# Optimization experiments

Measured on AMD Instinct MI355X. Metric: run time of the kernel, lower is better.

Reference implementation:

```python
import jax, jax.numpy as jnp
import numpy as np

N, E, B = 50000, 400000, 8
ND, ED, H, L = 32, 16, 128, 3

def setup_inputs() -> dict:
    key = jax.random.key(0)
    ks = jax.random.split(key, 32)
    s = 0.05
    inp = {
        'x': jax.random.normal(ks[0], (N, ND), jnp.float32),
        'edge_attr': jax.random.normal(ks[1], (E, ED), jnp.float32),
        'global_feature': jax.random.normal(ks[2], (B, 1), jnp.float32),
        'edge_index': jax.random.randint(ks[3], (2, E), 0, N, jnp.int64),
        'batch': jnp.sort(jax.random.randint(ks[4], (N,), 0, B, jnp.int64)),
        # embeddings
        'Wn': jax.random.normal(ks[5], (ND, H), jnp.float32) * s,
        'bn': jnp.zeros((H,), jnp.float32),
        'We': jax.random.normal(ks[6], (ED, H), jnp.float32) * s,
        'be': jnp.zeros((H,), jnp.float32),
        'Wg': jax.random.normal(ks[7], (1, H), jnp.float32) * s,
        'bg': jnp.zeros((H,), jnp.float32),
        # message-passing layers (stacked over L)
        'mW1': jax.random.normal(ks[8], (L, 3 * H, H), jnp.float32) * s,
        'mb1': jnp.zeros((L, H), jnp.float32),
        'mW2': jax.random.normal(ks[9], (L, H, H), jnp.float32) * s,
        'mb2': jnp.zeros((L, H), jnp.float32),
        'uW1': jax.random.normal(ks[10], (L, 2 * H, H), jnp.float32) * s,
        'ub1': jnp.zeros((L, H), jnp.float32),
        'uW2': jax.random.normal(ks[11], (L, H, H), jnp.float32) * s,
        'ub2': jnp.zeros((L, H), jnp.float32),
        # readout MLP
        'rW1': jax.random.normal(ks[12], (2 * H, H), jnp.float32) * s,
        'rb1': jnp.zeros((H,), jnp.float32),
        'rW2': jax.random.normal(ks[13], (H, H // 2), jnp.float32) * s,
        'rb2': jnp.zeros((H // 2,), jnp.float32),
        'rW3': jax.random.normal(ks[14], (H // 2, 1), jnp.float32) * s,
        'rb3': jnp.zeros((1,), jnp.float32),
    }
    return inp

def reference(x, edge_attr, global_feature, Wn, bn, We, be, Wg, bg,
              mW1, mb1, mW2, mb2, uW1, ub1, uW2, ub2,
              rW1, rb1, rW2, rb2, rW3, rb3, edge_index, batch):
    h = x @ Wn + bn                      # [N,H]
    e = edge_attr @ We + be              # [E,H]
    g = global_feature @ Wg + bg         # [B,H]
    src, dst = edge_index[0], edge_index[1]  # PyG: x_j=source, x_i=target, aggregate at target
    for l in range(L):
        m_in = jnp.concatenate([h[dst], h[src], e], axis=1)            # [E,3H]
        m = jax.nn.relu(m_in @ mW1[l] + mb1[l]) @ mW2[l] + mb2[l]       # [E,H]
        aggr = jax.ops.segment_sum(m, dst, num_segments=N)              # [N,H]
        u_in = jnp.concatenate([h, aggr], axis=1)                       # [N,2H]
        upd = jax.nn.relu(u_in @ uW1[l] + ub1[l]) @ uW2[l] + ub2[l]
        h = h + upd
    counts = jax.ops.segment_sum(jnp.ones((N,), h.dtype), batch, num_segments=B)
    pooled = jax.ops.segment_sum(h, batch, num_segments=B) / jnp.maximum(counts, 1.0)[:, None]
    final = jnp.concatenate([pooled, g], axis=1)                        # [B,2H]
    out = jax.nn.relu(final @ rW1 + rb1)
    out = jax.nn.relu(out @ rW2 + rb2)
    return out @ rW3 + rb3                                              # [B,1]
```

## Files before the change

kernel.cpp:

```cpp
#include <hip/hip_runtime.h>

#define NN 50000
#define NPAD 50048
#define NE 400000
#define NBATCH 8
#define NDIM 32
#define EDIM 16
#define H 128
#define NLAYERS 3
#define CHUNK_ELEMS 4096
#define NODE_CHUNKS 24
#define ZW_CHUNK 8192
#define NSB 196
#define ZEB 128

#define EMB_B 1563
#define DEG_B 1563
#define ZWB (NLAYERS * 8)
#define WEFB NLAYERS
#define WUB (NLAYERS * 257)
#define P1_B (EMB_B + DEG_B + ZWB + WEFB + WUB)
#define K2_B (NSB + NLAYERS + NLAYERS * NODE_CHUNKS)
#define ZDZS_B (NPAD / 64)
#define ZE_B (NE / ZEB)
#define ZZ_B (ZDZS_B + ZE_B)

typedef __attribute__((ext_vector_type(8))) __bf16 bf16x8;
typedef __attribute__((ext_vector_type(16))) float f32x16;
typedef __attribute__((ext_vector_type(8))) short short8;
typedef __attribute__((ext_vector_type(2))) float v2f;

__device__ __forceinline__ void block_sync_lds() {
  asm volatile("s_waitcnt lgkmcnt(0)\ns_barrier" ::: "memory");
}
__device__ __forceinline__ v2f bf2f(unsigned u) {
  v2f r;
  r.x = __uint_as_float(u << 16);
  r.y = __uint_as_float(u & 0xffff0000u);
  return r;
}

__global__ __launch_bounds__(256) void p1_kernel(
    const float* __restrict__ x, const float* __restrict__ Wn,
    const float* __restrict__ bn, __bf16* __restrict__ hb,
    const int* __restrict__ ei, int* __restrict__ deg,
    const float* __restrict__ mW1, __bf16* __restrict__ ZW,
    const float* __restrict__ mb1, const float* __restrict__ We,
    const float* __restrict__ be, float* __restrict__ Wef,
    float* __restrict__ bm, const float* __restrict__ uW1,
    const float* __restrict__ mW2, const float* __restrict__ mb2,
    float* __restrict__ Wu, float* __restrict__ va) {
  __shared__ __align__(16) float smem[NDIM * H + 32 * NDIM];
  int bi = blockIdx.x;
  int tid = threadIdx.x;
  if (bi < EMB_B) {
    float* Ws = smem;
    float* xs = smem + NDIM * H;
    int nbase = bi * 32;
    for (int f = tid; f < NDIM * H; f += 256) Ws[f] = Wn[f];
    for (int f = tid; f < 32 * NDIM; f += 256) {
      int gi = nbase * NDIM + f;
      xs[f] = (gi < NN * NDIM) ? x[gi] : 0.f;
    }
    __syncthreads();
    int j = tid & 127, g = tid >> 7;
    float b = bn[j];
    for (int nn = 0; nn < 16; ++nn) {
      int node = nbase + g * 16 + nn;
      if (node < NN) {
        float acc = b;
#pragma unroll
        for (int k = 0; k < NDIM; ++k)
          acc = fmaf(xs[(g * 16 + nn) * NDIM + k], Ws[k * H + j], acc);
        hb[(size_t)node * H + j] = (__bf16)acc;
      }
    }
  } else if (bi < EMB_B + DEG_B) {
    int e = (bi - EMB_B) * 256 + tid;
    if (e < NE) atomicAdd(&deg[ei[NE + e]], 1);
  } else if (bi < EMB_B + DEG_B + ZWB) {
    int bb = bi - EMB_B - DEG_B;
    int l = bb / 8;
    int c = bb % 8;
    const float* w1 = mW1 + (size_t)l * 384 * H;
    __bf16* dst = ZW + ((size_t)l * 8 + c) * ZW_CHUNK;
    for (int it = 0; it < 32; it += 4) {
      float wv[4];
#pragma unroll
      for (int q = 0; q < 4; ++q) {
        int flat = (it + q) * 256 + tid;
        int j = flat & 7;
        int lane = (flat >> 3) & 63;
        int nt = (flat >> 9) & 7;
        int k = c * 16 + ((lane >> 5) << 3) + j;
        int n = nt * 32 + (lane & 31);
        wv[q] = (n < 128) ? w1[(size_t)k * H + n]
                          : w1[(size_t)(128 + k) * H + (n - 128)];
      }
#pragma unroll
      for (int q = 0; q < 4; ++q) {
        int flat = (it + q) * 256 + tid;
        int hilo = flat >> 12;
        __bf16 hi = (__bf16)wv[q];
        __bf16 lo = (__bf16)(wv[q] - (float)hi);
        dst[flat] = hilo ? lo : hi;
      }
    }
  } else if (bi < EMB_B + DEG_B + ZWB + WEFB) {
    int l = bi - (EMB_B + DEG_B + ZWB);
    float* WeS = smem;
    float* beS = smem + 2048;
    for (int f = tid; f < EDIM * H; f += 256) WeS[f] = We[f];
    if (tid < 128) beS[tid] = be[tid];
    __syncthreads();
    if (tid < 128) {
      int n = tid;
      const float* w1 = mW1 + (size_t)l * 384 * H + (size_t)256 * H + n;
      float acc[EDIM];
#pragma unroll
      for (int i = 0; i < EDIM; ++i) acc[i] = 0.f;
      float accb = 0.f;
      for (int c = 0; c < H; c += 4) {
        float w0 = w1[(size_t)(c + 0) * H];
        float w1v = w1[(size_t)(c + 1) * H];
        float w2 = w1[(size_t)(c + 2) * H];
        float w3 = w1[(size_t)(c + 3) * H];
        accb = fmaf(beS[c + 0], w0, accb);
        accb = fmaf(beS[c + 1], w1v, accb);
        accb = fmaf(beS[c + 2], w2, accb);
        accb = fmaf(beS[c + 3], w3, accb);
#pragma unroll
        for (int i = 0; i < EDIM; ++i) {
          acc[i] = fmaf(WeS[i * H + c + 0], w0, acc[i]);
          acc[i] = fmaf(WeS[i * H + c + 1], w1v, acc[i]);
          acc[i] = fmaf(WeS[i * H + c + 2], w2, acc[i]);
          acc[i] = fmaf(WeS[i * H + c + 3], w3, acc[i]);
        }
      }
#pragma unroll
      for (int i = 0; i < EDIM; ++i)
        Wef[((size_t)l * EDIM + i) * H + n] = acc[i];
      bm[l * H + n] = mb1[l * H + n] + accb;
    }
  } else {
    int bb = bi - (EMB_B + DEG_B + ZWB + WEFB);
    int l = bb / 257;
    int r = bb % 257;
    int j = tid & 127, hf = tid >> 7;
    const float* u1 = uW1 + (size_t)l * 256 * H;
    if (r < 128) {
      if (tid < 128) Wu[((size_t)l * 256 + r) * H + j] = u1[(size_t)r * H + j];
    } else {
      float* rowS = smem;
      float* redS = smem + 128;
      if (tid < 128)
        rowS[tid] = (r < 256) ? mW2[((size_t)l * H + (r - 128)) * H + tid]
                              : mb2[l * H + tid];
      __syncthreads();
      int cb = hf * 64;
      float s0 = 0.f, s1 = 0.f, s2 = 0.f, s3 = 0.f;
      for (int c = 0; c < 64; c += 4) {
        float a0 = u1[(size_t)(128 + cb + c + 0) * H + j];
        float a1 = u1[(size_t)(128 + cb + c + 1) * H + j];
        float a2 = u1[(size_t)(128 + cb + c + 2) * H + j];
        float a3 = u1[(size_t)(128 + cb + c + 3) * H + j];
        s0 = fmaf(rowS[cb + c + 0], a0, s0);
        s1 = fmaf(rowS[cb + c + 1], a1, s1);
        s2 = fmaf(rowS[cb + c + 2], a2, s2);
        s3 = fmaf(rowS[cb + c + 3], a3, s3);
      }
      float s = (s0 + s1) + (s2 + s3);
      if (hf == 1) redS[j] = s;
      __syncthreads();
      if (hf == 0) {
        float tot = s + redS[j];
        if (r < 256) Wu[((size_t)l * 256 + r) * H + j] = tot;
        else va[l * H + j] = tot;
      }
    }
  }
}

__global__ __launch_bounds__(256) void k2_kernel(
    const int* __restrict__ deg, int* __restrict__ bsum,
    const float* __restrict__ Wef, __bf16* __restrict__ WefS,
    const float* __restrict__ Wu, const float* __restrict__ uW2,
    __bf16* __restrict__ WnS) {
  __shared__ int ws[4];
  int bi = blockIdx.x;
  int tid = threadIdx.x;
  if (bi < NSB) {
    int i = bi * 256 + tid;
    int lane = tid & 63, wid = tid >> 6;
    int v = (i < NN) ? deg[i] : 0;
#pragma unroll
    for (int off = 32; off; off >>= 1) v += __shfl_down(v, off);
    if (lane == 0) ws[wid] = v;
    __syncthreads();
    if (tid == 0) bsum[bi] = ws[0] + ws[1] + ws[2] + ws[3];
  } else if (bi < NSB + NLAYERS) {
    int l = bi - NSB;
    int nt = tid >> 6, lane = tid & 63;
    int n = nt * 32 + (lane & 31);
    int half = lane >> 5;
    const float* wl = Wef + (size_t)l * EDIM * H;
    __bf16* dst = WefS + (size_t)l * CHUNK_ELEMS;
#pragma unroll
    for (int j = 0; j < 8; ++j) {
      int k = half * 8 + j;
      float w = wl[(size_t)k * H + n];
      __bf16 hi = (__bf16)w;
      __bf16 lo = (__bf16)(w - (float)hi);
      dst[((0 * 4 + nt) * 64 + lane) * 8 + j] = hi;
      dst[((1 * 4 + nt) * 64 + lane) * 8 + j] = lo;
    }
  } else {
    int idx = bi - NSB - NLAYERS;
    int l = idx / NODE_CHUNKS;
    int c = idx % NODE_CHUNKS;
    int nt = tid >> 6, lane = tid & 63;
    int n = nt * 32 + (lane & 31);
    int half = lane >> 5;
    __bf16* dst = WnS + ((size_t)l * NODE_CHUNKS + c) * CHUNK_ELEMS;
#pragma unroll
    for (int j = 0; j < 8; ++j) {
      float w;
      if (c < 16) {
        int k = c * 16 + half * 8 + j;
        w = Wu[((size_t)l * 256 + k) * H + n];
      } else {
        int k = (c - 16) * 16 + half * 8 + j;
        w = uW2[((size_t)l * H + k) * H + n];
      }
      __bf16 hi = (__bf16)w;
      __bf16 lo = (__bf16)(w - (float)hi);
      dst[((0 * 4 + nt) * 64 + lane) * 8 + j] = hi;
      dst[((1 * 4 + nt) * 64 + lane) * 8 + j] = lo;
    }
  }
}

__global__ __launch_bounds__(256) void scan2_kernel(const int* __restrict__ bsum,
                                                    int* __restrict__ boff) {
  __shared__ int s[256];
  int t = threadIdx.x;
  int v = (t < NSB) ? bsum[t] : 0;
  s[t] = v;
  __syncthreads();
  for (int off = 1; off < 256; off <<= 1) {
    int u = (t >= off) ? s[t - off] : 0;
    __syncthreads();
    s[t] += u;
    __syncthreads();
  }
  if (t < NSB) boff[t] = s[t] - v;
}

__global__ __launch_bounds__(256) void scan3_kernel(const int* __restrict__ deg,
                                                    const int* __restrict__ boff,
                                                    int* __restrict__ cursor) {
  __shared__ int wsum[4], woff[4];
  int i = blockIdx.x * 256 + threadIdx.x;
  int lane = threadIdx.x & 63, wid = threadIdx.x >> 6;
  int orig = (i < NN) ? deg[i] : 0;
  int v = orig;
#pragma unroll
  for (int off = 1; off < 64; off <<= 1) {
    int u = __shfl_up(v, off);
    if (lane >= off) v += u;
  }
  if (lane == 63) wsum[wid] = v;
  __syncthreads();
  if (threadIdx.x == 0) {
    int r = 0;
#pragma unroll
    for (int w = 0; w < 4; ++w) {
      woff[w] = r;
      r += wsum[w];
    }
  }
  __syncthreads();
  if (i < NN) cursor[i] = (v - orig) + woff[wid] + boff[blockIdx.x];
}

__global__ __launch_bounds__(256) void scatter_kernel(
    const int* __restrict__ ei, int* __restrict__ cursor,
    int2* __restrict__ seSrt) {
  int e = blockIdx.x * 256 + threadIdx.x;
  if (e < NE) {
    int d = ei[NE + e];
    int pos = atomicAdd(&cursor[d], 1);
    seSrt[pos] = make_int2(ei[e], e);
  }
}

__global__ __launch_bounds__(256) void gather_ea_kernel(
    const float* __restrict__ ea, const int2* __restrict__ seSrt,
    __bf16* __restrict__ eaSrt) {
  int fl = blockIdx.x * 256 + threadIdx.x;
  if (fl < NE) {
    int e = seSrt[fl].y;
    const float4* ep = (const float4*)(ea + (size_t)e * EDIM);
    __bf16* op = eaSrt + (size_t)fl * EDIM;
#pragma unroll
    for (int q = 0; q < 4; ++q) {
      float4 v = ep[q];
      op[q * 4 + 0] = (__bf16)v.x;
      op[q * 4 + 1] = (__bf16)v.y;
      op[q * 4 + 2] = (__bf16)v.z;
      op[q * 4 + 3] = (__bf16)v.w;
    }
  }
}

__global__ __launch_bounds__(256) void zz_kernel(
    const __bf16* __restrict__ hb, const __bf16* __restrict__ ZW,
    const float* __restrict__ bm, __bf16* __restrict__ z,
    const __bf16* __restrict__ eaSrt, const __bf16* __restrict__ WefS,
    __bf16* __restrict__ zePre) {
  __shared__ __align__(16) __bf16 Bt[2][ZW_CHUNK];
  int bi = blockIdx.x;
  int tid = threadIdx.x;
  int wid = tid >> 6, lane = tid & 63, m = lane & 31, half = lane >> 5;
  if (bi < ZDZS_B) {
    int rg = wid & 1;
    int nh = wid >> 1;
    int nb = bi * 64;
    int row = nb + rg * 32 + m;
    const __bf16* aH = hb + (size_t)row * H + half * 8;
    const short8* gW = (const short8*)ZW;
    short8* sB0 = (short8*)&Bt[0][0];
    short8* sB1 = (short8*)&Bt[1][0];
#pragma unroll
    for (int q = 0; q < 4; ++q) sB0[tid + q * 256] = gW[tid + q * 256];
    short8 p0 = gW[1024 + tid], p1 = gW[1024 + tid + 256];
    short8 p2 = gW[1024 + tid + 512], p3 = gW[1024 + tid + 768];
    f32x16 acc[4];
#pragma unroll
    for (int ntl = 0; ntl < 4; ++ntl)
#pragma unroll
      for (int r = 0; r < 16; ++r) acc[ntl][r] = 0.f;
    bf16x8 a = *(const bf16x8*)aH;
    block_sync_lds();

    for (int s = 0; s < 8; ++s) {
      int buf = s & 1;
      bf16x8 na = a;
      if (s + 1 < 8) na = *(const bf16x8*)(aH + (s + 1) * 16);
      if (s + 1 < 8) {
        short8* sb = buf ? sB0 : sB1;
        sb[tid] = p0;
        sb[tid + 256] = p1;
        sb[tid + 512] = p2;
        sb[tid + 768] = p3;
        if (s + 2 < 8) {
          p0 = gW[(size_t)(s + 2) * 1024 + tid];
          p1 = gW[(size_t)(s + 2) * 1024 + tid + 256];
          p2 = gW[(size_t)(s + 2) * 1024 + tid + 512];
          p3 = gW[(size_t)(s + 2) * 1024 + tid + 768];
        }
      }
      const __bf16* bb = &Bt[buf][0];
#pragma unroll
      for (int ntl = 0; ntl < 4; ++ntl) {
        int nt = nh * 4 + ntl;
        bf16x8 bh = *(const bf16x8*)&bb[((0 * 8 + nt) * 64 + lane) * 8];
        bf16x8 bl = *(const bf16x8*)&bb[((1 * 8 + nt) * 64 + lane) * 8];
        acc[ntl] = __builtin_amdgcn_mfma_f32_32x32x16_bf16(a, bh, acc[ntl], 0, 0, 0);
        acc[ntl] = __builtin_amdgcn_mfma_f32_32x32x16_bf16(a, bl, acc[ntl], 0, 0, 0);
      }
      a = na;
      if (s + 1 < 8) block_sync_lds();
    }

    float bmv[4];
#pragma unroll
    for (int ntl = 0; ntl < 4; ++ntl) {
      int nt = nh * 4 + ntl;
      bmv[ntl] = (nt < 4) ? bm[nt * 32 + m] : 0.f;
    }
#pragma unroll
    for (int ntl = 0; ntl < 4; ++ntl) {
      int nt = nh * 4 + ntl;
#pragma unroll
      for (int r = 0; r < 16; ++r) {
        int rowi = (r & 3) + 8 * (r >> 2) + 4 * half;
        z[(size_t)(nb + rg * 32 + rowi) * 256 + nt * 32 + m] =
            (__bf16)(acc[ntl][r] + bmv[ntl]);
      }
    }
  } else {
    __bf16* Bf = &Bt[0][0];
    ((short8*)Bf)[tid] = ((const short8*)WefS)[tid];
    ((short8*)Bf)[tid + 256] = ((const short8*)WefS)[tid + 256];
    int ebase = (bi - ZDZS_B) * ZEB + wid * 32;
    bf16x8 a = *(const bf16x8*)(eaSrt + (size_t)(ebase + m) * EDIM + half * 8);
    f32x16 acc[4];
#pragma unroll
    for (int nt = 0; nt < 4; ++nt)
#pragma unroll
      for (int r = 0; r < 16; ++r) acc[nt][r] = 0.f;
    block_sync_lds();
#pragma unroll
    for (int nt = 0; nt < 4; ++nt) {
      bf16x8 bh = *(const bf16x8*)&Bf[((0 * 4 + nt) * 64 + lane) * 8];
      bf16x8 bl = *(const bf16x8*)&Bf[((1 * 4 + nt) * 64 + lane) * 8];
      acc[nt] = __builtin_amdgcn_mfma_f32_32x32x16_bf16(a, bh, acc[nt], 0, 0, 0);
      acc[nt] = __builtin_amdgcn_mfma_f32_32x32x16_bf16(a, bl, acc[nt], 0, 0, 0);
    }
#pragma unroll
    for (int nt = 0; nt < 4; ++nt) {
#pragma unroll
      for (int r = 0; r < 16; ++r) {
        int rowi = (r & 3) + 8 * (r >> 2) + 4 * half;
        zePre[(size_t)(ebase + rowi) * H + nt * 32 + m] = (__bf16)acc[nt][r];
      }
    }
  }
}

__global__ __launch_bounds__(256) void edge_aggr_kernel(
    const __bf16* __restrict__ z, const int2* __restrict__ seSrt,
    const int* __restrict__ cend, const __bf16* __restrict__ zePre,
    __bf16* __restrict__ aggrB) {
  int node = blockIdx.x * 4 + (threadIdx.x >> 6);
  int lane = threadIdx.x & 63;
  int c0 = lane * 2;
  int end = cend[node];
  int start = node ? cend[node - 1] : 0;
  v2f acc = {0.f, 0.f};
  if (start < end) {
    v2f zd = bf2f(*(const unsigned*)(z + (size_t)node * 256 + c0));
    int sArr[4];
#pragma unroll
    for (int p = 0; p < 4; ++p)
      if (start + p < end) sArr[p] = seSrt[start + p].x;
    for (int e0 = start; e0 < end; e0 += 4) {
      unsigned zsb[4], zeb[4];
#pragma unroll
      for (int p = 0; p < 4; ++p) {
        if (e0 + p < end) {
          zsb[p] = *(const unsigned*)(z + (size_t)sArr[p] * 256 + 128 + c0);
          zeb[p] = *(const unsigned*)(zePre + (size_t)(e0 + p) * H + c0);
        }
      }
#pragma unroll
      for (int p = 0; p < 4; ++p)
        if (e0 + 4 + p < end) sArr[p] = seSrt[e0 + 4 + p].x;
#pragma unroll
      for (int p = 0; p < 4; ++p) {
        if (e0 + p < end) {
          v2f t = zd + bf2f(zsb[p]) + bf2f(zeb[p]);
          acc.x += fmaxf(t.x, 0.f);
          acc.y += fmaxf(t.y, 0.f);
        }
      }
    }
  }
  union { __bf16 b[2]; unsigned u; } pk;
  pk.b[0] = (__bf16)acc.x;
  pk.b[1] = (__bf16)acc.y;
  *(unsigned*)(aggrB + (size_t)node * H + c0) = pk.u;
}

__global__ __launch_bounds__(256) void node_update_mfma_kernel(
    __bf16* __restrict__ hb, const __bf16* __restrict__ aggrB,
    const int* __restrict__ deg, const __bf16* __restrict__ WnS,
    const float* __restrict__ ub1, const float* __restrict__ va,
    const float* __restrict__ ub2) {
  __shared__ __align__(16) __bf16 Bt[2][CHUNK_ELEMS];
  __shared__ __bf16 hid[2][32][132];
  __shared__ float degS[64];
  int tid = threadIdx.x;
  int nb = blockIdx.x * 64;
  if (tid < 64) degS[tid] = (float)deg[nb + tid];
  int wid = tid >> 6, lane = tid & 63, m = lane & 31, half = lane >> 5;
  int rg = wid & 1;
  int nh = wid >> 1;
  int row = nb + rg * 32 + m;
  const __bf16* aHb = hb + (size_t)row * H + half * 8;
  const __bf16* aGb = aggrB + (size_t)row * H + half * 8;
  const short8* gW = (const short8*)WnS;
  short8* sB0 = (short8*)&Bt[0][0];
  short8* sB1 = (short8*)&Bt[1][0];
  sB0[tid] = gW[tid];
  sB0[tid + 256] = gW[tid + 256];
  short8 p0 = gW[512 + tid], p1 = gW[512 + tid + 256];
  float bv1[2], bva[2];
#pragma unroll
  for (int ntl = 0; ntl < 2; ++ntl) {
    int nt = nh * 2 + ntl;
    bv1[ntl] = ub1[nt * 32 + m];
    bva[ntl] = va[nt * 32 + m];
  }
  f32x16 acc[2];
#pragma unroll
  for (int ntl = 0; ntl < 2; ++ntl)
#pragma unroll
    for (int r = 0; r < 16; ++r) acc[ntl][r] = 0.f;
  bf16x8 acur = *(const bf16x8*)aHb;
  block_sync_lds();

  for (int s = 0; s < 16; ++s) {
    int buf = s & 1;
    bf16x8 anext = acur;
    if (s + 1 < 16) {
      int sp = s + 1;
      anext = (sp < 8) ? *(const bf16x8*)(aHb + sp * 16)
                       : *(const bf16x8*)(aGb + (sp - 8) * 16);
    }
    {
      short8* sb = buf ? sB0 : sB1;
      sb[tid] = p0;
      sb[tid + 256] = p1;
      if (s + 2 < NODE_CHUNKS) {
        p0 = gW[(size_t)(s + 2) * 512 + tid];
        p1 = gW[(size_t)(s + 2) * 512 + tid + 256];
      }
    }
    const __bf16* bb = &Bt[buf][0];
#pragma unroll
    for (int ntl = 0; ntl < 2; ++ntl) {
      int nt = nh * 2 + ntl;
      bf16x8 bh = *(const bf16x8*)&bb[((0 * 4 + nt) * 64 + lane) * 8];
      bf16x8 bl = *(const bf16x8*)&bb[((1 * 4 + nt) * 64 + lane) * 8];
      acc[ntl] = __builtin_amdgcn_mfma_f32_32x32x16_bf16(acur, bh, acc[ntl], 0, 0, 0);
      acc[ntl] = __builtin_amdgcn_mfma_f32_32x32x16_bf16(acur, bl, acc[ntl], 0, 0, 0);
    }
    acur = anext;
    block_sync_lds();
  }

#pragma unroll
  for (int ntl = 0; ntl < 2; ++ntl) {
    int nt = nh * 2 + ntl;
#pragma unroll
    for (int r = 0; r < 16; ++r) {
      int rowi = (r & 3) + 8 * (r >> 2) + 4 * half;
      float v = acc[ntl][r] + bv1[ntl] + degS[rg * 32 + rowi] * bva[ntl];
      hid[rg][rowi][nt * 32 + m] = (__bf16)fmaxf(v, 0.f);
      acc[ntl][r] = 0.f;
    }
  }
  block_sync_lds();

  for (int s = 16; s < NODE_CHUNKS; ++s) {
    int buf = s & 1;
    if (s + 1 < NODE_CHUNKS) {
      short8* sb = buf ? sB0 : sB1;
      sb[tid] = p0;
      sb[tid + 256] = p1;
      if (s + 2 < NODE_CHUNKS) {
        p0 = gW[(size_t)(s + 2) * 512 + tid];
        p1 = gW[(size_t)(s + 2) * 512 + tid + 256];
      }
    }
    bf16x8 ah = *(const bf16x8*)&hid[rg][m][(s - 16) * 16 + half * 8];
    const __bf16* bb = &Bt[buf][0];
#pragma unroll
    for (int ntl = 0; ntl < 2; ++ntl) {
      int nt = nh * 2 + ntl;
      bf16x8 bh = *(const bf16x8*)&bb[((0 * 4 + nt) * 64 + lane) * 8];
      bf16x8 bl = *(const bf16x8*)&bb[((1 * 4 + nt) * 64 + lane) * 8];
      acc[ntl] = __builtin_amdgcn_mfma_f32_32x32x16_bf16(ah, bh, acc[ntl], 0, 0, 0);
      acc[ntl] = __builtin_amdgcn_mfma_f32_32x32x16_bf16(ah, bl, acc[ntl], 0, 0, 0);
    }
    if (s + 1 < NODE_CHUNKS) block_sync_lds();
  }

#pragma unroll
  for (int ntl = 0; ntl < 2; ++ntl) {
    int nt = nh * 2 + ntl;
    float b2 = ub2[nt * 32 + m];
#pragma unroll
    for (int r = 0; r < 16; ++r) {
      int rowi = (r & 3) + 8 * (r >> 2) + 4 * half;
      size_t idx = (size_t)(nb + rg * 32 + rowi) * H + nt * 32 + m;
      float hv = (float)hb[idx];
      hb[idx] = (__bf16)(hv + acc[ntl][r] + b2);
    }
  }
}

__global__ __launch_bounds__(256) void pool_kernel(
    const __bf16* __restrict__ hb, const int* __restrict__ batch,
    float* __restrict__ pooled, int* __restrict__ counts) {
  __shared__ float pS[NBATCH * H];
  __shared__ int cS[NBATCH];
  int tid = threadIdx.x;
  for (int i = tid; i < NBATCH * H; i += 256) pS[i] = 0.f;
  if (tid < NBATCH) cS[tid] = 0;
  __syncthreads();
  int c = tid & 15;
  int r0 = tid >> 4;
  int nbase = blockIdx.x * 128;
  v2f acc4[4] = {{0.f, 0.f}, {0.f, 0.f}, {0.f, 0.f}, {0.f, 0.f}};
  int cnt = 0;
  int cur = -1;
#pragma unroll
  for (int i = 0; i < 8; ++i) {
    int n = nbase + i * 16 + r0;
    if (n >= NN) break;
    int b = batch[n];
    if (b != cur) {
      if (cur >= 0) {
#pragma unroll
        for (int q = 0; q < 4; ++q) {
          atomicAdd(&pS[cur * H + c * 8 + q * 2], acc4[q].x);
          atomicAdd(&pS[cur * H + c * 8 + q * 2 + 1], acc4[q].y);
          acc4[q].x = 0.f;
          acc4[q].y = 0.f;
        }
        if (c == 0) atomicAdd(&cS[cur], cnt);
        cnt = 0;
      }
      cur = b;
    }
    uint4 v = *(const uint4*)(hb + (size_t)n * H + c * 8);
    acc4[0] += bf2f(v.x);
    acc4[1] += bf2f(v.y);
    acc4[2] += bf2f(v.z);
    acc4[3] += bf2f(v.w);
    cnt++;
  }
  if (cur >= 0) {
#pragma unroll
    for (int q = 0; q < 4; ++q) {
      atomicAdd(&pS[cur * H + c * 8 + q * 2], acc4[q].x);
      atomicAdd(&pS[cur * H + c * 8 + q * 2 + 1], acc4[q].y);
    }
    if (c == 0) atomicAdd(&cS[cur], cnt);
  }
  __syncthreads();
  for (int i = tid; i < NBATCH * H; i += 256) {
    float v = pS[i];
    if (v != 0.f) unsafeAtomicAdd(&pooled[i], v);
  }
  if (tid < NBATCH) {
    int cv = cS[tid];
    if (cv) atomicAdd(&counts[tid], cv);
  }
}

__global__ __launch_bounds__(128) void readout_kernel(
    const float* __restrict__ pooled, const int* __restrict__ counts,
    const float* __restrict__ gf, const float* __restrict__ Wg,
    const float* __restrict__ bg, const float* __restrict__ rW1,
    const float* __restrict__ rb1, const float* __restrict__ rW2,
    const float* __restrict__ rb2, const float* __restrict__ rW3,
    const float* __restrict__ rb3, float* __restrict__ out) {
  __shared__ float fin[256];
  __shared__ float t1[128];
  __shared__ float t2[64];
  int j = threadIdx.x;
  int b = blockIdx.x;
  float cnt = (float)counts[b];
  if (cnt < 1.f) cnt = 1.f;
  fin[j] = pooled[b * H + j] / cnt;
  fin[H + j] = fmaf(gf[b], Wg[j], bg[j]);
  __syncthreads();
  float a = rb1[j];
  for (int k = 0; k < 256; ++k) a = fmaf(fin[k], rW1[k * H + j], a);
  t1[j] = fmaxf(a, 0.f);
  __syncthreads();
  if (j < 64) {
    float a2 = rb2[j];
    for (int k = 0; k < 128; ++k) a2 = fmaf(t1[k], rW2[k * 64 + j], a2);
    t2[j] = fmaxf(a2, 0.f);
  }
  __syncthreads();
  if (j < 64) {
    float p = t2[j] * rW3[j];
#pragma unroll
    for (int off = 32; off; off >>= 1) p += __shfl_down(p, off);
    if (j == 0) out[b] = p + rb3[0];
  }
}

extern "C" void kernel_launch(void* const* d_in, const int* in_sizes, int n_in,
                              void* d_out, int out_size, void* d_ws, size_t ws_size,
                              hipStream_t stream) {
  const float* x   = (const float*)d_in[0];
  const float* ea  = (const float*)d_in[1];
  const float* gf  = (const float*)d_in[2];
  const int*   ei  = (const int*)d_in[3];
  const int*   bat = (const int*)d_in[4];
  const float* Wn  = (const float*)d_in[5];
  const float* bn  = (const float*)d_in[6];
  const float* We  = (const float*)d_in[7];
  const float* be  = (const float*)d_in[8];
  const float* Wg  = (const float*)d_in[9];
  const float* bg  = (const float*)d_in[10];
  const float* mW1 = (const float*)d_in[11];
  const float* mb1 = (const float*)d_in[12];
  const float* mW2 = (const float*)d_in[13];
  const float* mb2 = (const float*)d_in[14];
  const float* uW1 = (const float*)d_in[15];
  const float* ub1 = (const float*)d_in[16];
  const float* uW2 = (const float*)d_in[17];
  const float* ub2 = (const float*)d_in[18];
  const float* rW1 = (const float*)d_in[19];
  const float* rb1 = (const float*)d_in[20];
  const float* rW2 = (const float*)d_in[21];
  const float* rb2 = (const float*)d_in[22];
  const float* rW3 = (const float*)d_in[23];
  const float* rb3 = (const float*)d_in[24];

  char* p = (char*)d_ws;
  __bf16* hb     = (__bf16*)p; p += (size_t)NPAD * H * 2;
  __bf16* aggrB  = (__bf16*)p; p += (size_t)NPAD * H * 2;
  __bf16* z      = (__bf16*)p; p += (size_t)NPAD * 256 * 2;
  __bf16* zePre  = (__bf16*)p; p += (size_t)NE * H * 2;
  __bf16* eaSrt  = (__bf16*)p; p += (size_t)NE * EDIM * 2;
  int2*   seSrt  = (int2*)p;   p += (size_t)NE * 8;
  __bf16* ZW     = (__bf16*)p; p += (size_t)NLAYERS * 8 * ZW_CHUNK * 2;
  __bf16* WnS    = (__bf16*)p; p += (size_t)NLAYERS * NODE_CHUNKS * CHUNK_ELEMS * 2;
  __bf16* WefS   = (__bf16*)p; p += (size_t)NLAYERS * CHUNK_ELEMS * 2;
  float*  Wef    = (float*)p;  p += (size_t)NLAYERS * EDIM * H * 4;
  float*  bm     = (float*)p;  p += (size_t)NLAYERS * H * 4;
  float*  Wu     = (float*)p;  p += (size_t)NLAYERS * 256 * H * 4;
  float*  va     = (float*)p;  p += (size_t)NLAYERS * H * 4;
  int*    deg    = (int*)p;    p += (size_t)NPAD * 4;
  int*    cursor = (int*)p;    p += (size_t)NPAD * 4;
  int*    bsum   = (int*)p;    p += 256 * 4;
  int*    boff   = (int*)p;    p += 256 * 4;
  float*  pooled = (float*)p;  p += (size_t)NBATCH * H * 4;
  int*    counts = (int*)p;    p += 64;

  hipMemsetAsync(deg, 0, (size_t)NPAD * 4, stream);
  hipMemsetAsync(cursor, 0, (size_t)NPAD * 4, stream);
  hipMemsetAsync(pooled, 0, (size_t)NBATCH * H * 4, stream);
  hipMemsetAsync(counts, 0, 64, stream);

  p1_kernel<<<P1_B, 256, 0, stream>>>(x, Wn, bn, hb, ei, deg, mW1, ZW, mb1, We,
                                      be, Wef, bm, uW1, mW2, mb2, Wu, va);
  k2_kernel<<<K2_B, 256, 0, stream>>>(deg, bsum, Wef, WefS, Wu, uW2, WnS);
  scan2_kernel<<<1, 256, 0, stream>>>(bsum, boff);
  scan3_kernel<<<NSB, 256, 0, stream>>>(deg, boff, cursor);
  scatter_kernel<<<(NE + 255) / 256, 256, 0, stream>>>(ei, cursor, seSrt);
  gather_ea_kernel<<<(NE + 255) / 256, 256, 0, stream>>>(ea, seSrt, eaSrt);

  for (int l = 0; l < NLAYERS; ++l) {
    zz_kernel<<<ZZ_B, 256, 0, stream>>>(
        hb, ZW + (size_t)l * 8 * ZW_CHUNK, bm + (size_t)l * H, z,
        eaSrt, WefS + (size_t)l * CHUNK_ELEMS, zePre);
    edge_aggr_kernel<<<NPAD / 4, 256, 0, stream>>>(
        z, seSrt, cursor, zePre, aggrB);
    node_update_mfma_kernel<<<NPAD / 64, 256, 0, stream>>>(
        hb, aggrB, deg, WnS + (size_t)l * NODE_CHUNKS * CHUNK_ELEMS,
        ub1 + (size_t)l * H, va + (size_t)l * H, ub2 + (size_t)l * H);
  }

  pool_kernel<<<NPAD / 128, 256, 0, stream>>>(hb, bat, pooled, counts);
  readout_kernel<<<NBATCH, 128, 0, stream>>>(pooled, counts, gf, Wg, bg, rW1,
                                             rb1, rW2, rb2, rW3, rb3,
                                             (float*)d_out);
}
```

Measured before the change: 498.6 us.

## Fuse edge-attr gather into scatter, fold Wef packing into p1, slim sorted-edge array

The scatter kernel now reads each edge's attributes directly and writes the bf16 row to its sorted position, which removes the separate gather_ea kernel and the indirect reload it did. The sorted-edge buffer shrinks from int2 (src, edge id) to an int holding only src, so edge_aggr reads half as many index bytes per edge. The Wef hi/lo bf16 packing moves into p1 through shared memory, dropping a global fp32 round trip and some k2 blocks. The node embedding caches its weight column in registers and reads x with float4 loads. The scatter now does scattered 32-byte writes per edge in exchange.

```diff
diff --git a/kernel.cpp b/kernel.cpp
--- a/kernel.cpp
+++ b/kernel.cpp
@@ -20,7 +20,7 @@
 #define WEFB NLAYERS
 #define WUB (NLAYERS * 257)
 #define P1_B (EMB_B + DEG_B + ZWB + WEFB + WUB)
-#define K2_B (NSB + NLAYERS + NLAYERS * NODE_CHUNKS)
+#define K2_B (NSB + NLAYERS * NODE_CHUNKS)
 #define ZDZS_B (NPAD / 64)
 #define ZE_B (NE / ZEB)
 #define ZZ_B (ZDZS_B + ZE_B)
@@ -46,7 +46,7 @@
     const int* __restrict__ ei, int* __restrict__ deg,
     const float* __restrict__ mW1, __bf16* __restrict__ ZW,
     const float* __restrict__ mb1, const float* __restrict__ We,
-    const float* __restrict__ be, float* __restrict__ Wef,
+    const float* __restrict__ be, __bf16* __restrict__ WefS,
     float* __restrict__ bm, const float* __restrict__ uW1,
     const float* __restrict__ mW2, const float* __restrict__ mb2,
     float* __restrict__ Wu, float* __restrict__ va) {
@@ -64,14 +64,23 @@
     }
     __syncthreads();
     int j = tid & 127, g = tid >> 7;
+    float wcol[NDIM];
+#pragma unroll
+    for (int k = 0; k < NDIM; ++k) wcol[k] = Ws[k * H + j];
     float b = bn[j];
     for (int nn = 0; nn < 16; ++nn) {
       int node = nbase + g * 16 + nn;
       if (node < NN) {
         float acc = b;
-#pragma unroll
-        for (int k = 0; k < NDIM; ++k)
-          acc = fmaf(xs[(g * 16 + nn) * NDIM + k], Ws[k * H + j], acc);
+        const float4* xv = (const float4*)&xs[(g * 16 + nn) * NDIM];
+#pragma unroll
+        for (int k4 = 0; k4 < NDIM / 4; ++k4) {
+          float4 v = xv[k4];
+          acc = fmaf(v.x, wcol[k4 * 4 + 0], acc);
+          acc = fmaf(v.y, wcol[k4 * 4 + 1], acc);
+          acc = fmaf(v.z, wcol[k4 * 4 + 2], acc);
+          acc = fmaf(v.w, wcol[k4 * 4 + 3], acc);
+        }
         hb[(size_t)node * H + j] = (__bf16)acc;
       }
     }
@@ -110,6 +119,7 @@
     int l = bi - (EMB_B + DEG_B + ZWB);
     float* WeS = smem;
     float* beS = smem + 2048;
+    float* wefT = smem + 2176;
     for (int f = tid; f < EDIM * H; f += 256) WeS[f] = We[f];
     if (tid < 128) beS[tid] = be[tid];
     __syncthreads();
@@ -138,9 +148,24 @@
         }
       }
 #pragma unroll
-      for (int i = 0; i < EDIM; ++i)
-        Wef[((size_t)l * EDIM + i) * H + n] = acc[i];
+      for (int i = 0; i < EDIM; ++i) wefT[i * H + n] = acc[i];
       bm[l * H + n] = mb1[l * H + n] + accb;
+    }
+    __syncthreads();
+    {
+      int nt = tid >> 6, lane = tid & 63;
+      int n = nt * 32 + (lane & 31);
+      int half = lane >> 5;
+      __bf16* dst = WefS + (size_t)l * CHUNK_ELEMS;
+#pragma unroll
+      for (int j = 0; j < 8; ++j) {
+        int k = half * 8 + j;
+        float w = wefT[k * H + n];
+        __bf16 hi = (__bf16)w;
+        __bf16 lo = (__bf16)(w - (float)hi);
+        dst[((0 * 4 + nt) * 64 + lane) * 8 + j] = hi;
+        dst[((1 * 4 + nt) * 64 + lane) * 8 + j] = lo;
+      }
     }
   } else {
     int bb = bi - (EMB_B + DEG_B + ZWB + WEFB);
@@ -183,7 +208,6 @@
 
 __global__ __launch_bounds__(256) void k2_kernel(
     const int* __restrict__ deg, int* __restrict__ bsum,
-    const float* __restrict__ Wef, __bf16* __restrict__ WefS,
     const float* __restrict__ Wu, const float* __restrict__ uW2,
     __bf16* __restrict__ WnS) {
   __shared__ int ws[4];
@@ -198,24 +222,8 @@
     if (lane == 0) ws[wid] = v;
     __syncthreads();
     if (tid == 0) bsum[bi] = ws[0] + ws[1] + ws[2] + ws[3];
-  } else if (bi < NSB + NLAYERS) {
-    int l = bi - NSB;
-    int nt = tid >> 6, lane = tid & 63;
-    int n = nt * 32 + (lane & 31);
-    int half = lane >> 5;
-    const float* wl = Wef + (size_t)l * EDIM * H;
-    __bf16* dst = WefS + (size_t)l * CHUNK_ELEMS;
-#pragma unroll
-    for (int j = 0; j < 8; ++j) {
-      int k = half * 8 + j;
-      float w = wl[(size_t)k * H + n];
-      __bf16 hi = (__bf16)w;
-      __bf16 lo = (__bf16)(w - (float)hi);
-      dst[((0 * 4 + nt) * 64 + lane) * 8 + j] = hi;
-      dst[((1 * 4 + nt) * 64 + lane) * 8 + j] = lo;
-    }
   } else {
-    int idx = bi - NSB - NLAYERS;
+    int idx = bi - NSB;
     int l = idx / NODE_CHUNKS;
     int c = idx % NODE_CHUNKS;
     int nt = tid >> 6, lane = tid & 63;
@@ -285,31 +293,28 @@
 
 __global__ __launch_bounds__(256) void scatter_kernel(
     const int* __restrict__ ei, int* __restrict__ cursor,
-    int2* __restrict__ seSrt) {
+    int* __restrict__ srcSrt, const float* __restrict__ ea,
+    __bf16* __restrict__ eaSrt) {
   int e = blockIdx.x * 256 + threadIdx.x;
   if (e < NE) {
     int d = ei[NE + e];
+    int s = ei[e];
+    const float4* ep = (const float4*)(ea + (size_t)e * EDIM);
+    float4 v0 = ep[0], v1 = ep[1], v2 = ep[2], v3 = ep[3];
     int pos = atomicAdd(&cursor[d], 1);
-    seSrt[pos] = make_int2(ei[e], e);
-  }
-}
-
-__global__ __launch_bounds__(256) void gather_ea_kernel(
-    const float* __restrict__ ea, const int2* __restrict__ seSrt,
-    __bf16* __restrict__ eaSrt) {
-  int fl = blockIdx.x * 256 + threadIdx.x;
-  if (fl < NE) {
-    int e = seSrt[fl].y;
-    const float4* ep = (const float4*)(ea + (size_t)e * EDIM);
-    __bf16* op = eaSrt + (size_t)fl * EDIM;
-#pragma unroll
-    for (int q = 0; q < 4; ++q) {
-      float4 v = ep[q];
-      op[q * 4 + 0] = (__bf16)v.x;
-      op[q * 4 + 1] = (__bf16)v.y;
-      op[q * 4 + 2] = (__bf16)v.z;
-      op[q * 4 + 3] = (__bf16)v.w;
-    }
+    srcSrt[pos] = s;
+    union { __bf16 b[16]; uint4 u[2]; } pk;
+    pk.b[0] = (__bf16)v0.x;  pk.b[1] = (__bf16)v0.y;
+    pk.b[2] = (__bf16)v0.z;  pk.b[3] = (__bf16)v0.w;
+    pk.b[4] = (__bf16)v1.x;  pk.b[5] = (__bf16)v1.y;
+    pk.b[6] = (__bf16)v1.z;  pk.b[7] = (__bf16)v1.w;
+    pk.b[8] = (__bf16)v2.x;  pk.b[9] = (__bf16)v2.y;
+    pk.b[10] = (__bf16)v2.z; pk.b[11] = (__bf16)v2.w;
+    pk.b[12] = (__bf16)v3.x; pk.b[13] = (__bf16)v3.y;
+    pk.b[14] = (__bf16)v3.z; pk.b[15] = (__bf16)v3.w;
+    uint4* op = (uint4*)(eaSrt + (size_t)pos * EDIM);
+    op[0] = pk.u[0];
+    op[1] = pk.u[1];
   }
 }
 
@@ -420,7 +425,7 @@
 }
 
 __global__ __launch_bounds__(256) void edge_aggr_kernel(
-    const __bf16* __restrict__ z, const int2* __restrict__ seSrt,
+    const __bf16* __restrict__ z, const int* __restrict__ srcSrt,
     const int* __restrict__ cend, const __bf16* __restrict__ zePre,
     __bf16* __restrict__ aggrB) {
   int node = blockIdx.x * 4 + (threadIdx.x >> 6);
@@ -434,7 +439,7 @@
     int sArr[4];
 #pragma unroll
     for (int p = 0; p < 4; ++p)
-      if (start + p < end) sArr[p] = seSrt[start + p].x;
+      if (start + p < end) sArr[p] = srcSrt[start + p];
     for (int e0 = start; e0 < end; e0 += 4) {
       unsigned zsb[4], zeb[4];
 #pragma unroll
@@ -446,7 +451,7 @@
       }
 #pragma unroll
       for (int p = 0; p < 4; ++p)
-        if (e0 + 4 + p < end) sArr[p] = seSrt[e0 + 4 + p].x;
+        if (e0 + 4 + p < end) sArr[p] = srcSrt[e0 + 4 + p];
 #pragma unroll
       for (int p = 0; p < 4; ++p) {
         if (e0 + p < end) {
@@ -712,11 +717,10 @@
   __bf16* z      = (__bf16*)p; p += (size_t)NPAD * 256 * 2;
   __bf16* zePre  = (__bf16*)p; p += (size_t)NE * H * 2;
   __bf16* eaSrt  = (__bf16*)p; p += (size_t)NE * EDIM * 2;
-  int2*   seSrt  = (int2*)p;   p += (size_t)NE * 8;
+  int*    srcSrt = (int*)p;    p += (size_t)NE * 4;
   __bf16* ZW     = (__bf16*)p; p += (size_t)NLAYERS * 8 * ZW_CHUNK * 2;
   __bf16* WnS    = (__bf16*)p; p += (size_t)NLAYERS * NODE_CHUNKS * CHUNK_ELEMS * 2;
   __bf16* WefS   = (__bf16*)p; p += (size_t)NLAYERS * CHUNK_ELEMS * 2;
-  float*  Wef    = (float*)p;  p += (size_t)NLAYERS * EDIM * H * 4;
   float*  bm     = (float*)p;  p += (size_t)NLAYERS * H * 4;
   float*  Wu     = (float*)p;  p += (size_t)NLAYERS * 256 * H * 4;
   float*  va     = (float*)p;  p += (size_t)NLAYERS * H * 4;
@@ -733,19 +737,19 @@
   hipMemsetAsync(counts, 0, 64, stream);
 
   p1_kernel<<<P1_B, 256, 0, stream>>>(x, Wn, bn, hb, ei, deg, mW1, ZW, mb1, We,
-                                      be, Wef, bm, uW1, mW2, mb2, Wu, va);
-  k2_kernel<<<K2_B, 256, 0, stream>>>(deg, bsum, Wef, WefS, Wu, uW2, WnS);
+                                      be, WefS, bm, uW1, mW2, mb2, Wu, va);
+  k2_kernel<<<K2_B, 256, 0, stream>>>(deg, bsum, Wu, uW2, WnS);
   scan2_kernel<<<1, 256, 0, stream>>>(bsum, boff);
   scan3_kernel<<<NSB, 256, 0, stream>>>(deg, boff, cursor);
-  scatter_kernel<<<(NE + 255) / 256, 256, 0, stream>>>(ei, cursor, seSrt);
-  gather_ea_kernel<<<(NE + 255) / 256, 256, 0, stream>>>(ea, seSrt, eaSrt);
+  scatter_kernel<<<(NE + 255) / 256, 256, 0, stream>>>(ei, cursor, srcSrt, ea,
+                                                       eaSrt);
 
   for (int l = 0; l < NLAYERS; ++l) {
     zz_kernel<<<ZZ_B, 256, 0, stream>>>(
         hb, ZW + (size_t)l * 8 * ZW_CHUNK, bm + (size_t)l * H, z,
         eaSrt, WefS + (size_t)l * CHUNK_ELEMS, zePre);
     edge_aggr_kernel<<<NPAD / 4, 256, 0, stream>>>(
-        z, seSrt, cursor, zePre, aggrB);
+        z, srcSrt, cursor, zePre, aggrB);
     node_update_mfma_kernel<<<NPAD / 64, 256, 0, stream>>>(
         hb, aggrB, deg, WnS + (size_t)l * NODE_CHUNKS * CHUNK_ELEMS,
         ub1 + (size_t)l * H, va + (size_t)l * H, ub2 + (size_t)l * H);
```

Measured after the change: 489.3 us. No clear change (-1.9%).
